# Kernel tuning notes

Measured on AMD Instinct MI355X. Metric: run time of the kernel, lower is better.

## Reference

```python
import jax, jax.numpy as jnp
import numpy as np

SEGMENT_LENGTHS = (768, 1536, 3072, 6144, 12288)
DILATED_RATIOS = (1, 2, 4, 8, 16)
NUM_HEADS = 12
NEG_INF = -1e9


def _layer_norm(x, g, b, eps=1e-5):
    mu = jnp.mean(x, axis=-1, keepdims=True)
    var = jnp.mean((x - mu) ** 2, axis=-1, keepdims=True)
    return (x - mu) * jax.lax.rsqrt(var + eps) * g + b


def _dilated_branch(q, k, v, w, r):
    # q,k,v: (B, L, H, Dh); segment length w, dilation ratio r (w % r == 0)
    B, L, H, Dh = q.shape
    Lp = -(-L // w) * w
    n, m = Lp // w, w // r
    gsz = -(-H // r)  # head-group size (heads padded up to a multiple of r in LongNet)
    offs = jnp.arange(H) // gsz  # per-head token offset within each r-block
    oh = jax.nn.one_hot(offs, r, dtype=q.dtype)  # (H, r)

    def gather(t):
        t = jnp.pad(t, ((0, 0), (0, Lp - L), (0, 0), (0, 0)))
        t = t.reshape(B, n, m, r, H, Dh)  # segments of w = m blocks of r
        return jnp.einsum('bnmrhd,hr->bnmhd', t, oh)  # each head picks its offset

    qi, ki, vi = gather(q), gather(k), gather(v)
    s = jnp.einsum('bnihd,bnjhd->bnhij', qi * (Dh ** -0.5), ki)  # (B,n,H,m,m)
    lse = jax.scipy.special.logsumexp(s, axis=-1)  # (B,n,H,m)
    o = jnp.einsum('bnhij,bnjhd->bnihd', jax.nn.softmax(s, axis=-1), vi)
    # scatter back to dense token positions; uncovered slots get 0 / -inf lse
    o_full = jnp.einsum('bnmhd,hr->bnmrhd', o, oh).reshape(B, Lp, H, Dh)
    lse = jnp.transpose(lse, (0, 1, 3, 2))  # (B,n,m,H)
    lse_full = jnp.where(oh.T[None, None, None] > 0, lse[:, :, :, None, :], NEG_INF)
    lse_full = lse_full.reshape(B, Lp, H)
    return o_full[:, :L], lse_full[:, :L]


def _dilated_attention(q, k, v):
    outs, lses = [], []
    for w, r in zip(SEGMENT_LENGTHS, DILATED_RATIOS):
        o, l = _dilated_branch(q, k, v, w, r)
        outs.append(o)
        lses.append(l)
    lse = jnp.stack(lses)  # (n_branch, B, L, H)
    wts = jnp.exp(lse - lse.max(0))
    wts = wts / wts.sum(0)  # softmax-combine branches by their lse (LongNet recombination)
    return (jnp.stack(outs) * wts[..., None]).sum(0)  # (B, L, H, Dh)


def _forward(x, patch_w, patch_b, cls_token, pos_embed,
             ln1_g, ln1_b, wq, bq, wk, bk, wv, bv, wo, bo,
             ln2_g, ln2_b, w1, b1, w2, b2, normf_g, normf_b, head_w, head_b):
    B, Cin, D, Hs, Ws = x.shape
    E = patch_w.shape[0]
    pd, ph, pw = patch_w.shape[2], patch_w.shape[3], patch_w.shape[4]
    # non-overlapping 3D patch embed (Conv3d with stride == kernel)
    xp = x.reshape(B, Cin, D // pd, pd, Hs // ph, ph, Ws // pw, pw)
    tok = jnp.einsum('bcxpyqzr,ecpqr->bxyze', xp, patch_w).reshape(B, -1, E) + patch_b
    tok = tok + pos_embed[:, 1:]
    cls = cls_token + pos_embed[:, :1]
    h = jnp.concatenate([jnp.broadcast_to(cls, (B, 1, E)), tok], axis=1)
    L = h.shape[1]
    Dh = E // NUM_HEADS
    depth = wq.shape[0]
    for i in range(depth):  # pre-LN transformer layers with LongNet dilated attention
        hn = _layer_norm(h, ln1_g[i], ln1_b[i])
        q = (hn @ wq[i] + bq[i]).reshape(B, L, NUM_HEADS, Dh)
        k = (hn @ wk[i] + bk[i]).reshape(B, L, NUM_HEADS, Dh)
        v = (hn @ wv[i] + bv[i]).reshape(B, L, NUM_HEADS, Dh)
        a = _dilated_attention(q, k, v).reshape(B, L, E)
        h = h + a @ wo[i] + bo[i]
        hn = _layer_norm(h, ln2_g[i], ln2_b[i])
        h = h + jax.nn.gelu(hn @ w1[i] + b1[i], approximate=False) @ w2[i] + b2[i]
    h = _layer_norm(h, normf_g, normf_b)
    return h[:, 0] @ head_w + head_b  # (B, num_classes)


def setup_inputs() -> dict:
    key = jax.random.key(0)
    ks = jax.random.split(key, 12)
    B, E, depth, ncls = 2, 768, 2, 1000
    D, Hs, Ws = 48, 256, 256
    N = (D // 4) * (Hs // 16) * (Ws // 16)  # 3072 patches
    f32 = jnp.float32
    s = 0.02
    return {
        'x': jax.random.normal(ks[0], (B, 1, D, Hs, Ws), f32),
        'patch_w': jax.random.normal(ks[1], (E, 1, 4, 16, 16), f32) * s,
        'patch_b': jnp.zeros((E,), f32),
        'cls_token': jax.random.normal(ks[2], (1, 1, E), f32) * s,
        'pos_embed': jax.random.normal(ks[3], (1, N + 1, E), f32) * s,
        'ln1_g': jnp.ones((depth, E), f32),
        'ln1_b': jnp.zeros((depth, E), f32),
        'wq': jax.random.normal(ks[4], (depth, E, E), f32) * s,
        'bq': jnp.zeros((depth, E), f32),
        'wk': jax.random.normal(ks[5], (depth, E, E), f32) * s,
        'bk': jnp.zeros((depth, E), f32),
        'wv': jax.random.normal(ks[6], (depth, E, E), f32) * s,
        'bv': jnp.zeros((depth, E), f32),
        'wo': jax.random.normal(ks[7], (depth, E, E), f32) * s,
        'bo': jnp.zeros((depth, E), f32),
        'ln2_g': jnp.ones((depth, E), f32),
        'ln2_b': jnp.zeros((depth, E), f32),
        'w1': jax.random.normal(ks[8], (depth, E, 4 * E), f32) * s,
        'b1': jnp.zeros((depth, 4 * E), f32),
        'w2': jax.random.normal(ks[9], (depth, 4 * E, E), f32) * s,
        'b2': jnp.zeros((depth, E), f32),
        'normf_g': jnp.ones((E,), f32),
        'normf_b': jnp.zeros((E,), f32),
        'head_w': jax.random.normal(ks[10], (E, ncls), f32) * s,
        'head_b': jnp.zeros((ncls,), f32),
    }


def reference(x, patch_w, patch_b, cls_token, pos_embed,
              ln1_g, ln1_b, wq, bq, wk, bk, wv, bv, wo, bo,
              ln2_g, ln2_b, w1, b1, w2, b2, normf_g, normf_b, head_w, head_b):
    return _forward(x, patch_w, patch_b, cls_token, pos_embed,
                    ln1_g, ln1_b, wq, bq, wk, bk, wv, bv, wo, bo,
                    ln2_g, ln2_b, w1, b1, w2, b2, normf_g, normf_b, head_w, head_b)
```

## Files before the change

### kernel.cpp

```cpp
#include <hip/hip_runtime.h>
#include <math.h>

#define TOK_L 3073
#define EMB 768
#define NH 12
#define DH 64
#define BATCH 2
#define QKVS 2304
#define HSZ ((size_t)BATCH * TOK_L * EMB)
#define MHC ((size_t)BATCH * TOK_L * NH)

typedef __bf16 bf16;
typedef __bf16 v8bf __attribute__((ext_vector_type(8)));
typedef __bf16 v4bf __attribute__((ext_vector_type(4)));
typedef float  v4f  __attribute__((ext_vector_type(4)));
typedef unsigned int v4u __attribute__((ext_vector_type(4)));

__device__ __forceinline__ v8bf zero8() {
    v8bf v;
    #pragma unroll
    for (int i = 0; i < 8; i++) v[i] = (bf16)0.f;
    return v;
}
__device__ __forceinline__ v4f zero4() {
    v4f v; v[0] = 0.f; v[1] = 0.f; v[2] = 0.f; v[3] = 0.f; return v;
}
__device__ __forceinline__ float gelu_f(float x) {
    return 0.5f * x * (1.0f + erff(x * 0.70710678118654752f));
}
__device__ __forceinline__ void gload16(const bf16* g, bf16* l) {
    __builtin_amdgcn_global_load_lds(
        (const __attribute__((address_space(1))) void*)g,
        (__attribute__((address_space(3))) void*)l, 16, 0, 0);
}

__device__ __forceinline__ void convT_tile(const float* __restrict__ src,
                                           bf16* __restrict__ dst,
                                           int K, int N, int tx, int ty)
{
    __shared__ float t[32][33];
    int n0 = tx * 32, k0 = ty * 32;
    int r = threadIdx.x >> 3, c4 = (threadIdx.x & 7) * 4;
    float4 v = *(const float4*)(src + (size_t)(k0 + r) * N + n0 + c4);
    t[r][c4 + 0] = v.x; t[r][c4 + 1] = v.y; t[r][c4 + 2] = v.z; t[r][c4 + 3] = v.w;
    __syncthreads();
    v4bf o;
    o[0] = (bf16)t[c4 + 0][r]; o[1] = (bf16)t[c4 + 1][r];
    o[2] = (bf16)t[c4 + 2][r]; o[3] = (bf16)t[c4 + 3][r];
    *(v4bf*)(dst + (size_t)(n0 + r) * K + k0 + c4) = o;
}

__global__ __launch_bounds__(256) void prep_weights(
    const float* __restrict__ wq, const float* __restrict__ wk,
    const float* __restrict__ wv, const float* __restrict__ wo,
    const float* __restrict__ w1, const float* __restrict__ w2,
    const float* __restrict__ patch_w,
    bf16* __restrict__ qkv_t0, bf16* __restrict__ wo_t0,
    bf16* __restrict__ w1_t, bf16* __restrict__ w2_t, bf16* __restrict__ pw_b)
{
    int bid = blockIdx.x;
    if (bid >= 13824) {
        int i = ((bid - 13824) * 256 + threadIdx.x) * 4;
        float4 v = *(const float4*)(patch_w + i);
        v4bf o; o[0] = (bf16)v.x; o[1] = (bf16)v.y; o[2] = (bf16)v.z; o[3] = (bf16)v.w;
        *(v4bf*)(pw_b + i) = o;
        return;
    }
    int layer = bid / 6912, t = bid % 6912;
    if (t < 1728) {
        int m = t / 576, tt = t % 576;
        const float* src = (m == 0 ? wq : m == 1 ? wk : wv) + (size_t)layer * 589824;
        bf16* dst = qkv_t0 + (size_t)layer * QKVS * 768 + (size_t)m * 589824;
        convT_tile(src, dst, 768, 768, tt % 24, tt / 24);
    } else if (t < 2304) {
        int tt = t - 1728;
        convT_tile(wo + (size_t)layer * 589824, wo_t0 + (size_t)layer * 589824,
                   768, 768, tt % 24, tt / 24);
    } else if (t < 4608) {
        int tt = t - 2304;
        convT_tile(w1 + (size_t)layer * 2359296, w1_t + (size_t)layer * 2359296,
                   768, 3072, tt % 96, tt / 96);
    } else {
        int tt = t - 4608;
        convT_tile(w2 + (size_t)layer * 2359296, w2_t + (size_t)layer * 2359296,
                   3072, 768, tt % 24, tt / 24);
    }
}

__global__ __launch_bounds__(256) void prep_small(const float* __restrict__ bq,
    const float* __restrict__ bk, const float* __restrict__ bv, float* __restrict__ d,
    const float* __restrict__ cls, const float* __restrict__ pos, float* __restrict__ h)
{
    int i = blockIdx.x * 256 + threadIdx.x;
    if (i < 2 * QKVS) {
        int layer = i / QKVS, j = i % QKVS;
        const float* s = (j < 768) ? bq : (j < 1536) ? bk : bv;
        d[i] = s[(size_t)layer * 768 + (j & 767)];
    }
    if (i < 2 * 768) {
        int b = i / 768, e = i % 768;
        h[(size_t)b * TOK_L * EMB + e] = cls[e] + pos[e];
    }
}

__global__ __launch_bounds__(256) void gather_patches(const float* __restrict__ x,
                                                      bf16* __restrict__ Xp) {
    int p = blockIdx.x;
    int b = p / 3072, pp = p % 3072;
    int px = pp >> 8, py = (pp >> 4) & 15, pz = pp & 15;
    for (int k = threadIdx.x; k < 1024; k += 256) {
        int pd = k >> 8, ph = (k >> 4) & 15, pw = k & 15;
        size_t src = ((size_t)(b * 48 + px * 4 + pd)) * 65536
                   + (size_t)(py * 16 + ph) * 256 + (size_t)(pz * 16 + pw);
        Xp[(size_t)p * 1024 + k] = (bf16)x[src];
    }
}

__device__ __forceinline__ void remap_tile(int NX, int MY, int G, int& xo, int& yo)
{
    int id = blockIdx.x + NX * blockIdx.y;
    int nwg = NX * MY;
    int xcd = id & 7, j = id >> 3;
    int q = nwg >> 3, r = nwg & 7;
    int n = xcd * q + (xcd < r ? xcd : r) + j;
    int full = MY / G;
    int bpg = NX * G;
    int nf = full * bpg;
    if (n < nf) {
        int gi = n / bpg, w = n - gi * bpg;
        int xi = w / G;
        xo = xi; yo = gi * G + (w - xi * G);
    } else {
        int t = MY - full * G;
        int w = n - nf;
        int xi = w / t;
        xo = xi; yo = full * G + (w - xi * t);
    }
}

template<int BN>
__global__ __launch_bounds__(256) void gemm_bf16(
    const bf16* __restrict__ A, const bf16* __restrict__ Bt,
    const float* __restrict__ bias, float* __restrict__ Cf,
    bf16* __restrict__ Cb, int M, int N, int K, int flags,
    const float* __restrict__ pos, int G)
{
    __shared__ bf16 As[2][128 * 32];
    __shared__ bf16 Bs[2][BN * 32];
    const int tid = threadIdx.x;
    const int lane = tid & 63, wid = tid >> 6;
    const int ln15 = lane & 15, q4 = lane >> 4;
    int xo, yo;
    remap_tile(gridDim.x, gridDim.y, G, xo, yo);
    const int m0 = yo * 128, n0 = xo * BN;
    const int wm = (wid & 1) * 64, wn = (wid >> 1) * (BN / 2);
    const int srow = lane >> 2;
    const int schunk = (lane & 3) * 8;
    const int NF = BN / 32;

    v4f acc[4][NF];
    #pragma unroll
    for (int i = 0; i < 4; i++)
        #pragma unroll
        for (int j = 0; j < NF; j++) acc[i][j] = zero4();

    const int NT = K >> 5;
    auto stage = [&](int kt, int bi) {
        const int k0 = kt << 5;
        #pragma unroll
        for (int i = 0; i < 2; i++) {
            int rg = wid * 32 + i * 16;
            int gm = m0 + rg + srow; if (gm >= M) gm = M - 1;
            gload16(A + (size_t)gm * K + k0 + schunk, &As[bi][rg * 32]);
        }
        if (BN == 128) {
            #pragma unroll
            for (int i = 0; i < 2; i++) {
                int rg = wid * 32 + i * 16;
                gload16(Bt + (size_t)(n0 + rg + srow) * K + k0 + schunk, &Bs[bi][rg * 32]);
            }
        } else {
            int rg = wid * 16;
            gload16(Bt + (size_t)(n0 + rg + srow) * K + k0 + schunk, &Bs[bi][rg * 32]);
        }
    };

    stage(0, 0);
    __syncthreads();

    for (int kt = 0; kt < NT; kt++) {
        const int cur = kt & 1;
        if (kt + 1 < NT) stage(kt + 1, cur ^ 1);
        v8bf af[4], bfr[NF];
        #pragma unroll
        for (int mt = 0; mt < 4; mt++)
            af[mt] = *(const v8bf*)(&As[cur][(wm + mt * 16 + ln15) * 32 + q4 * 8]);
        #pragma unroll
        for (int nt = 0; nt < NF; nt++)
            bfr[nt] = *(const v8bf*)(&Bs[cur][(wn + nt * 16 + ln15) * 32 + q4 * 8]);
        #pragma unroll
        for (int mt = 0; mt < 4; mt++)
            #pragma unroll
            for (int nt = 0; nt < NF; nt++)
                acc[mt][nt] = __builtin_amdgcn_mfma_f32_16x16x32_bf16(af[mt], bfr[nt], acc[mt][nt], 0, 0, 0);
        __syncthreads();
    }
    #pragma unroll
    for (int mt = 0; mt < 4; mt++) {
        #pragma unroll
        for (int nt = 0; nt < NF; nt++) {
            #pragma unroll
            for (int g = 0; g < 4; g++) {
                int row = m0 + wm + mt * 16 + q4 * 4 + g;
                if (row >= M) continue;
                int col = n0 + wn + nt * 16 + ln15;
                float v = acc[mt][nt][g] + bias[col];
                if (flags & 2) v = gelu_f(v);
                size_t crow;
                if (flags & 4) {
                    int rowp = row % 3072;
                    crow = (size_t)(row + row / 3072 + 1);
                    v += pos[(size_t)(rowp + 1) * EMB + col];
                } else crow = (size_t)row;
                size_t ci = crow * (size_t)N + col;
                if (flags & 8) Cb[ci] = (bf16)v;
                else { if (flags & 1) v += Cf[ci]; Cf[ci] = v; }
            }
        }
    }
}

__global__ __launch_bounds__(256) void layernorm_kernel(
    const float* __restrict__ x, const float* __restrict__ g,
    const float* __restrict__ bb, bf16* __restrict__ y, int nrows)
{
    int row = blockIdx.x;
    if (row >= nrows) return;
    int tid = threadIdx.x;
    const float* xr = x + (size_t)row * EMB;
    float v0 = xr[tid], v1 = xr[tid + 256], v2 = xr[tid + 512];
    __shared__ float red[256];
    red[tid] = v0 + v1 + v2;
    __syncthreads();
    for (int o = 128; o > 0; o >>= 1) { if (tid < o) red[tid] += red[tid + o]; __syncthreads(); }
    float mu = red[0] * (1.f / 768.f);
    __syncthreads();
    float d0 = v0 - mu, d1 = v1 - mu, d2 = v2 - mu;
    red[tid] = d0 * d0 + d1 * d1 + d2 * d2;
    __syncthreads();
    for (int o = 128; o > 0; o >>= 1) { if (tid < o) red[tid] += red[tid + o]; __syncthreads(); }
    float rs = rsqrtf(red[0] * (1.f / 768.f) + 1e-5f);
    bf16* yr = y + (size_t)row * EMB;
    yr[tid]       = (bf16)(d0 * rs * g[tid]       + bb[tid]);
    yr[tid + 256] = (bf16)(d1 * rs * g[tid + 256] + bb[tid + 256]);
    yr[tid + 512] = (bf16)(d2 * rs * g[tid + 512] + bb[tid + 512]);
}

__global__ __launch_bounds__(256) void pack_vt(const bf16* __restrict__ qkv,
                                               bf16* __restrict__ Vt)
{
    __shared__ bf16 t[64 * 65];
    int yy = blockIdx.y;
    int br, seg;
    if (yy < 5)       { br = 0; seg = yy; }
    else if (yy < 8)  { br = 1; seg = yy - 5; }
    else if (yy < 10) { br = 2; seg = yy - 8; }
    else if (yy == 10){ br = 3; seg = 0; }
    else              { br = 4; seg = 0; }
    const int r = 1 << br, w = 768 << br;
    const int gsz = (NH + r - 1) / r;
    const int bh = blockIdx.z;
    const int b = bh / NH, hd = bh % NH;
    const int off = hd / gsz;
    const int kbase = seg * w + off;
    const int kt = blockIdx.x;
    const int tid = threadIdx.x;
    const int dq = (tid & 7) * 8;
    #pragma unroll
    for (int p = 0; p < 2; p++) {
        int jl = (tid >> 3) + p * 32;
        int pk = kbase + (kt * 64 + jl) * r;
        v8bf val = (pk < TOK_L)
            ? *(const v8bf*)(qkv + (size_t)(b * TOK_L + pk) * QKVS + 1536 + hd * DH + dq)
            : zero8();
        #pragma unroll
        for (int i = 0; i < 8; i++) t[jl * 65 + dq + i] = val[i];
    }
    __syncthreads();
    #pragma unroll
    for (int p = 0; p < 2; p++) {
        int d = (tid >> 3) + p * 32;
        int kk = (tid & 7) * 8;
        v8bf o;
        #pragma unroll
        for (int i = 0; i < 8; i++) o[i] = t[(kk + i) * 65 + d];
        *(v8bf*)(Vt + ((size_t)(yy * 24 + bh) * 64 + d) * 768 + kt * 64 + kk) = o;
    }
}

__global__ __launch_bounds__(256) void attn_mfma(
    const bf16* __restrict__ qkv, const bf16* __restrict__ Vt,
    bf16* __restrict__ oac, bf16* __restrict__ obr, float* __restrict__ lse5)
{
    __shared__ bf16 kl[2 * 4096];
    const int tid = threadIdx.x;
    const int lane = tid & 63, wid = tid >> 6;
    const int ln15 = lane & 15, q4 = lane >> 4;
    const int bid = blockIdx.x;
    const int xcd = bid & 7, rest = bid >> 3;
    const int slot = rest / 6, t = rest - slot * 6;
    const int g = (slot << 3) | xcd;
    const int yy = g / 24, bh = g - yy * 24;
    int br, seg;
    if (yy < 5)       { br = 0; seg = yy; }
    else if (yy < 8)  { br = 1; seg = yy - 5; }
    else if (yy < 10) { br = 2; seg = yy - 8; }
    else if (yy == 10){ br = 3; seg = 0; }
    else              { br = 4; seg = 0; }
    const int r = 1 << br, w = 768 << br;
    const int gsz = (NH + r - 1) / r;
    const int b = bh / NH, hd = bh % NH;
    const int off = hd / gsz;
    const int sbase = seg * w + off;
    if (sbase + (t * 128) * r >= TOK_L) return;

    int n_valid = (TOK_L - sbase + r - 1) / r;
    if (n_valid > 768) n_valid = 768;
    const int kt_lim = (n_valid + 63) >> 6;
    const float pad_add = (float)(768 - n_valid);
    const int qoff = t * 128 + wid * 32;
    const bool wactive = (sbase + qoff * r) < TOK_L;

    const bf16* qb_ = qkv + hd * DH;
    const bf16* kb_ = qkv + 768 + hd * DH;

    const int swz = (ln15 & 7) * 8;

    auto stageK = [&](int ktv, int bufi) {
        #pragma unroll
        for (int p = 0; p < 2; p++) {
            int row = (tid >> 3) + p * 32;
            int pk = sbase + (ktv * 64 + row) * r;
            if (pk >= TOK_L) pk = 0;
            int colsw = ((tid & 7) ^ ((tid >> 3) & 7)) * 8;
            gload16(kb_ + (size_t)(b * TOK_L + pk) * QKVS + colsw,
                    kl + bufi * 4096 + wid * 512 + p * 2048);
        }
    };

    v8bf qf[2][2];
    #pragma unroll
    for (int mt = 0; mt < 2; mt++) {
        int pq = sbase + (qoff + mt * 16 + ln15) * r;
        #pragma unroll
        for (int ks = 0; ks < 2; ks++) {
            v8bf qv = (pq < TOK_L)
                ? *(const v8bf*)(qb_ + (size_t)(b * TOK_L + pq) * QKVS + ks * 32 + q4 * 8)
                : zero8();
            #pragma unroll
            for (int i = 0; i < 8; i++) qv[i] = (bf16)((float)qv[i] * 0.125f);
            qf[mt][ks] = qv;
        }
    }
    v4f o[2][4];
    float lsum[2];
    #pragma unroll
    for (int mt = 0; mt < 2; mt++) {
        lsum[mt] = 0.f;
        #pragma unroll
        for (int dt = 0; dt < 4; dt++) o[mt][dt] = zero4();
    }

    const bf16* vtb = Vt + (size_t)(yy * 24 + bh) * 64 * 768;

    stageK(0, 0);
    __syncthreads();

    for (int kt = 0; kt < kt_lim; kt++) {
        const int cur = kt & 1;
        if (kt + 1 < kt_lim) stageK(kt + 1, cur ^ 1);
        if (wactive) {
            const bf16* klc = kl + cur * 4096;
            v8bf kf[4][2];
            #pragma unroll
            for (int nt = 0; nt < 4; nt++)
                #pragma unroll
                for (int ks = 0; ks < 2; ks++)
                    kf[nt][ks] = *(const v8bf*)(klc + (nt * 16 + ln15) * 64
                                                + ((ks * 32 + q4 * 8) ^ swz));
            unsigned int paw[2][2][4];
            #pragma unroll
            for (int mt = 0; mt < 2; mt++) {
                v4f s[4];
                #pragma unroll
                for (int nt = 0; nt < 4; nt++) {
                    s[nt] = __builtin_amdgcn_mfma_f32_16x16x32_bf16(kf[nt][0], qf[mt][0], zero4(), 0, 0, 0);
                    s[nt] = __builtin_amdgcn_mfma_f32_16x16x32_bf16(kf[nt][1], qf[mt][1], s[nt], 0, 0, 0);
                }
                unsigned int W[4][2];
                float ls = 0.f;
                #pragma unroll
                for (int nt = 0; nt < 4; nt++) {
                    int kb = kt * 64 + nt * 16 + q4 * 4;
                    float p0 = (kb + 0 < n_valid) ? __expf(s[nt][0]) : 0.f;
                    float p1 = (kb + 1 < n_valid) ? __expf(s[nt][1]) : 0.f;
                    float p2 = (kb + 2 < n_valid) ? __expf(s[nt][2]) : 0.f;
                    float p3 = (kb + 3 < n_valid) ? __expf(s[nt][3]) : 0.f;
                    ls += (p0 + p1) + (p2 + p3);
                    asm("v_cvt_pk_bf16_f32 %0, %1, %2" : "=v"(W[nt][0]) : "v"(p0), "v"(p1));
                    asm("v_cvt_pk_bf16_f32 %0, %1, %2" : "=v"(W[nt][1]) : "v"(p2), "v"(p3));
                }
                lsum[mt] += ls;
                #pragma unroll
                for (int ks = 0; ks < 2; ks++) {
                    #pragma unroll
                    for (int h = 0; h < 2; h++) {
                        unsigned int a = W[2 * ks][h], c = W[2 * ks + 1][h];
                        asm("v_permlane32_swap_b32 %0, %1" : "+v"(a), "+v"(c));
                        asm("v_permlane16_swap_b32 %0, %1" : "+v"(a), "+v"(c));
                        paw[mt][ks][h]     = a;
                        paw[mt][ks][2 + h] = c;
                    }
                }
            }
            #pragma unroll
            for (int ks = 0; ks < 2; ks++) {
                v8bf vf[4];
                #pragma unroll
                for (int dt = 0; dt < 4; dt++)
                    vf[dt] = *(const v8bf*)(vtb + (size_t)(dt * 16 + ln15) * 768 + kt * 64 + ks * 32 + q4 * 8);
                #pragma unroll
                for (int mt = 0; mt < 2; mt++) {
                    v4u pw = { paw[mt][ks][0], paw[mt][ks][1], paw[mt][ks][2], paw[mt][ks][3] };
                    v8bf pa = __builtin_bit_cast(v8bf, pw);
                    #pragma unroll
                    for (int dt = 0; dt < 4; dt++)
                        o[mt][dt] = __builtin_amdgcn_mfma_f32_16x16x32_bf16(pa, vf[dt], o[mt][dt], 0, 0, 0);
                }
            }
        }
        __syncthreads();
    }
    if (!wactive) return;

    float lf[2];
    #pragma unroll
    for (int mt = 0; mt < 2; mt++) {
        float l = lsum[mt];
        l += __shfl_xor(l, 16, 64);
        l += __shfl_xor(l, 32, 64);
        l += pad_add;
        lf[mt] = l;
        if (q4 == 0) {
            int pq = sbase + (qoff + mt * 16 + ln15) * r;
            if (pq < TOK_L)
                lse5[(size_t)br * MHC + (size_t)(b * TOK_L + pq) * NH + hd] = __logf(l);
        }
    }

    bf16* od = (br == 0) ? oac : obr + (size_t)(br - 1) * HSZ;
    #pragma unroll
    for (int mt = 0; mt < 2; mt++) {
        #pragma unroll
        for (int g2 = 0; g2 < 4; g2++) {
            float l = __shfl(lf[mt], q4 * 4 + g2, 64);
            int row = mt * 16 + q4 * 4 + g2;
            int pq = sbase + (qoff + row) * r;
            if (pq >= TOK_L) continue;
            float linv = 1.f / l;
            #pragma unroll
            for (int dt = 0; dt < 4; dt++)
                od[(size_t)(b * TOK_L + pq) * EMB + hd * DH + dt * 16 + ln15] =
                    (bf16)(o[mt][dt][g2] * linv);
        }
    }
}

__global__ __launch_bounds__(256) void attn_combine(
    const bf16* __restrict__ oac, const bf16* __restrict__ obr,
    const float* __restrict__ lse5, bf16* __restrict__ outb)
{
    size_t e = (size_t)blockIdx.x * 256 + threadIdx.x;
    if (e >= HSZ) return;
    size_t g = e >> 6;
    int h = (int)(g % NH);
    int p = (int)((g / NH) % TOK_L);
    float l0 = lse5[g];
    float m = l0;
    float lv[4];
    bool cov[4];
    #pragma unroll
    for (int j = 0; j < 4; j++) {
        int r = 2 << j;
        int gsz = (NH + r - 1) / r;
        cov[j] = ((p & (r - 1)) == (h / gsz));
        if (cov[j]) {
            lv[j] = lse5[(size_t)(j + 1) * MHC + g];
            m = fmaxf(m, lv[j]);
        }
    }
    float w0 = __expf(l0 - m);
    float wsum = w0;
    float acc = w0 * (float)oac[e];
    #pragma unroll
    for (int j = 0; j < 4; j++) {
        if (cov[j]) {
            float wj = __expf(lv[j] - m);
            wsum += wj;
            acc = fmaf(wj, (float)obr[(size_t)j * HSZ + e], acc);
        }
    }
    outb[e] = (bf16)(acc / wsum);
}

__global__ __launch_bounds__(256) void head_kernel(
    const bf16* __restrict__ hn, const float* __restrict__ hw,
    const float* __restrict__ hb, float* __restrict__ out)
{
    int b = blockIdx.y;
    int c = blockIdx.x * 256 + threadIdx.x;
    __shared__ float srow[EMB];
    for (int e = threadIdx.x; e < EMB; e += 256)
        srow[e] = (float)hn[(size_t)b * TOK_L * EMB + e];
    __syncthreads();
    if (c < 1000) {
        float acc = hb[c];
        for (int e = 0; e < EMB; e++)
            acc = fmaf(srow[e], hw[(size_t)e * 1000 + c], acc);
        out[b * 1000 + c] = acc;
    }
}

extern "C" void kernel_launch(void* const* d_in, const int* in_sizes, int n_in,
                              void* d_out, int out_size, void* d_ws, size_t ws_size,
                              hipStream_t stream)
{
    const float* x       = (const float*)d_in[0];
    const float* patch_w = (const float*)d_in[1];
    const float* patch_b = (const float*)d_in[2];
    const float* cls_tok = (const float*)d_in[3];
    const float* pos_emb = (const float*)d_in[4];
    const float* ln1_g   = (const float*)d_in[5];
    const float* ln1_b   = (const float*)d_in[6];
    const float* wq      = (const float*)d_in[7];
    const float* bq      = (const float*)d_in[8];
    const float* wk      = (const float*)d_in[9];
    const float* bk      = (const float*)d_in[10];
    const float* wv      = (const float*)d_in[11];
    const float* bv      = (const float*)d_in[12];
    const float* wo      = (const float*)d_in[13];
    const float* bo      = (const float*)d_in[14];
    const float* ln2_g   = (const float*)d_in[15];
    const float* ln2_b   = (const float*)d_in[16];
    const float* w1      = (const float*)d_in[17];
    const float* b1      = (const float*)d_in[18];
    const float* w2      = (const float*)d_in[19];
    const float* b2      = (const float*)d_in[20];
    const float* normf_g = (const float*)d_in[21];
    const float* normf_b = (const float*)d_in[22];
    const float* head_w  = (const float*)d_in[23];
    const float* head_b  = (const float*)d_in[24];
    float* out = (float*)d_out;

    char* wp = (char*)d_ws;
    auto alloc = [&](size_t bytes) { char* r = wp; wp += (bytes + 255) & ~(size_t)255; return r; };
    float* h    = (float*)alloc(HSZ * 4);
    bf16*  hn   = (bf16*)alloc(HSZ * 2);
    bf16*  QKV  = (bf16*)alloc((size_t)BATCH * TOK_L * QKVS * 2);
    bf16*  oac  = (bf16*)alloc(HSZ * 2);
    float* lse5 = (float*)alloc(5 * MHC * 4);
    bf16*  Vt   = (bf16*)alloc((size_t)12 * 24 * 64 * 768 * 2);
    bf16*  mid  = (bf16*)alloc(4 * HSZ * 2);
    bf16*  obr  = mid;
    bf16*  Xp   = mid;

    bf16*  qkv_t0 = (bf16*)alloc((size_t)2 * QKVS * 768 * 2);
    bf16*  wo_t0  = (bf16*)alloc((size_t)2 * 768 * 768 * 2);
    bf16*  w1_t   = (bf16*)alloc((size_t)2 * 3072 * 768 * 2);
    bf16*  w2_t   = (bf16*)alloc((size_t)2 * 768 * 3072 * 2);
    bf16*  pw_b   = (bf16*)alloc((size_t)768 * 1024 * 2);
    float* bqkv   = (float*)alloc((size_t)2 * QKVS * 4);

    const int M = BATCH * TOK_L;
    const int MT = (M + 127) / 128;

    prep_weights<<<dim3(14592), 256, 0, stream>>>(wq, wk, wv, wo, w1, w2, patch_w,
                                                  qkv_t0, wo_t0, w1_t, w2_t, pw_b);
    prep_small<<<dim3(18), 256, 0, stream>>>(bq, bk, bv, bqkv, cls_tok, pos_emb, h);

    gather_patches<<<dim3(BATCH * 3072), 256, 0, stream>>>(x, Xp);
    gemm_bf16<64><<<dim3(12, 48), 256, 0, stream>>>(Xp, pw_b, patch_b, h, nullptr,
                                                    BATCH * 3072, 768, 1024, 4, pos_emb, 8);

    for (int layer = 0; layer < 2; layer++) {
        size_t bOff  = (size_t)layer * 768;
        size_t b1Off = (size_t)layer * 3072;
        bf16* qt   = qkv_t0 + (size_t)layer * QKVS * 768;
        bf16* wo_t = wo_t0 + (size_t)layer * 589824;

        layernorm_kernel<<<dim3(M), 256, 0, stream>>>(h, ln1_g + bOff, ln1_b + bOff, hn, M);
        gemm_bf16<128><<<dim3(18, MT), 256, 0, stream>>>(hn, qt, bqkv + (size_t)layer * QKVS,
                                                         nullptr, QKV, M, QKVS, 768, 8, nullptr, 8);

        pack_vt<<<dim3(12, 12, 24), 256, 0, stream>>>(QKV, Vt);
        attn_mfma<<<dim3(1728), 256, 0, stream>>>(QKV, Vt, oac, obr, lse5);
        attn_combine<<<dim3((unsigned)((HSZ + 255) / 256)), 256, 0, stream>>>(oac, obr, lse5, hn);

        gemm_bf16<64><<<dim3(12, MT), 256, 0, stream>>>(hn, wo_t, bo + bOff, h, nullptr,
                                                        M, 768, 768, 1, nullptr, 8);

        layernorm_kernel<<<dim3(M), 256, 0, stream>>>(h, ln2_g + bOff, ln2_b + bOff, hn, M);
        gemm_bf16<128><<<dim3(24, MT), 256, 0, stream>>>(hn, w1_t + (size_t)layer * 2359296, b1 + b1Off,
                                                         nullptr, mid, M, 3072, 768, 8 | 2, nullptr, 8);
        gemm_bf16<64><<<dim3(12, MT), 256, 0, stream>>>(mid, w2_t + (size_t)layer * 2359296, b2 + bOff,
                                                        h, nullptr, M, 768, 3072, 1, nullptr, 4);
    }

    layernorm_kernel<<<dim3(M), 256, 0, stream>>>(h, normf_g, normf_b, hn, M);
    head_kernel<<<dim3(4, BATCH), 256, 0, stream>>>(hn, head_w, head_b, out);
}
```

Before: 972.6 us.

## Double GEMM M-tile to 256 rows and replace syncthreads with explicit vmcnt waits

The bf16 GEMM tile grows from 128 to 256 rows. Each wave now owns 128x64 (BN=128) or 64x64 (BN=64) of the output, which raises MFMA work per shared-memory fragment load and halves grid rows. The loop drops __syncthreads and instead waits on outstanding global loads with s_waitcnt vmcnt counts, then issues raw s_barrier with sched barriers, so the next tile's prefetch overlaps the current compute. The larger tile doubles LDS use and raises accumulator register pressure, and halving the number of blocks may underfill the GPU's CUs. The hand-counted vmcnt values must match the number of loads each stage issues.

```diff
diff --git a/kernel.cpp b/kernel.cpp
--- a/kernel.cpp
+++ b/kernel.cpp
@@ -145,31 +145,32 @@
     bf16* __restrict__ Cb, int M, int N, int K, int flags,
     const float* __restrict__ pos, int G)
 {
-    __shared__ bf16 As[2][128 * 32];
+    __shared__ bf16 As[2][256 * 32];
     __shared__ bf16 Bs[2][BN * 32];
     const int tid = threadIdx.x;
     const int lane = tid & 63, wid = tid >> 6;
     const int ln15 = lane & 15, q4 = lane >> 4;
     int xo, yo;
     remap_tile(gridDim.x, gridDim.y, G, xo, yo);
-    const int m0 = yo * 128, n0 = xo * BN;
-    const int wm = (wid & 1) * 64, wn = (wid >> 1) * (BN / 2);
+    const int m0 = yo * 256, n0 = xo * BN;
+    constexpr int MTW = (BN == 128) ? 8 : 4;
+    const int wm = (BN == 128) ? (wid & 1) * 128 : wid * 64;
+    const int wn = (BN == 128) ? (wid >> 1) * 64 : 0;
     const int srow = lane >> 2;
     const int schunk = (lane & 3) * 8;
-    const int NF = BN / 32;
-
-    v4f acc[4][NF];
-    #pragma unroll
-    for (int i = 0; i < 4; i++)
-        #pragma unroll
-        for (int j = 0; j < NF; j++) acc[i][j] = zero4();
+
+    v4f acc[MTW][4];
+    #pragma unroll
+    for (int i = 0; i < MTW; i++)
+        #pragma unroll
+        for (int j = 0; j < 4; j++) acc[i][j] = zero4();
 
     const int NT = K >> 5;
     auto stage = [&](int kt, int bi) {
         const int k0 = kt << 5;
         #pragma unroll
-        for (int i = 0; i < 2; i++) {
-            int rg = wid * 32 + i * 16;
+        for (int i = 0; i < 4; i++) {
+            int rg = wid * 64 + i * 16;
             int gm = m0 + rg + srow; if (gm >= M) gm = M - 1;
             gload16(A + (size_t)gm * K + k0 + schunk, &As[bi][rg * 32]);
         }
@@ -186,29 +187,38 @@
     };
 
     stage(0, 0);
-    __syncthreads();
 
     for (int kt = 0; kt < NT; kt++) {
         const int cur = kt & 1;
-        if (kt + 1 < NT) stage(kt + 1, cur ^ 1);
-        v8bf af[4], bfr[NF];
-        #pragma unroll
-        for (int mt = 0; mt < 4; mt++)
+        if (kt + 1 < NT) {
+            stage(kt + 1, cur ^ 1);
+            if (BN == 128) asm volatile("s_waitcnt vmcnt(6)" ::: "memory");
+            else           asm volatile("s_waitcnt vmcnt(5)" ::: "memory");
+        } else {
+            asm volatile("s_waitcnt vmcnt(0)" ::: "memory");
+        }
+        __builtin_amdgcn_sched_barrier(0);
+        __builtin_amdgcn_s_barrier();
+        __builtin_amdgcn_sched_barrier(0);
+
+        v8bf af[MTW], bfr[4];
+        #pragma unroll
+        for (int mt = 0; mt < MTW; mt++)
             af[mt] = *(const v8bf*)(&As[cur][(wm + mt * 16 + ln15) * 32 + q4 * 8]);
         #pragma unroll
-        for (int nt = 0; nt < NF; nt++)
+        for (int nt = 0; nt < 4; nt++)
             bfr[nt] = *(const v8bf*)(&Bs[cur][(wn + nt * 16 + ln15) * 32 + q4 * 8]);
         #pragma unroll
-        for (int mt = 0; mt < 4; mt++)
-            #pragma unroll
-            for (int nt = 0; nt < NF; nt++)
+        for (int mt = 0; mt < MTW; mt++)
+            #pragma unroll
+            for (int nt = 0; nt < 4; nt++)
                 acc[mt][nt] = __builtin_amdgcn_mfma_f32_16x16x32_bf16(af[mt], bfr[nt], acc[mt][nt], 0, 0, 0);
-        __syncthreads();
-    }
-    #pragma unroll
-    for (int mt = 0; mt < 4; mt++) {
-        #pragma unroll
-        for (int nt = 0; nt < NF; nt++) {
+        __builtin_amdgcn_s_barrier();
+    }
+    #pragma unroll
+    for (int mt = 0; mt < MTW; mt++) {
+        #pragma unroll
+        for (int nt = 0; nt < 4; nt++) {
             #pragma unroll
             for (int g = 0; g < 4; g++) {
                 int row = m0 + wm + mt * 16 + q4 * 4 + g;
@@ -582,15 +592,15 @@
     float* bqkv   = (float*)alloc((size_t)2 * QKVS * 4);
 
     const int M = BATCH * TOK_L;
-    const int MT = (M + 127) / 128;
+    const int MT2 = (M + 255) / 256;
 
     prep_weights<<<dim3(14592), 256, 0, stream>>>(wq, wk, wv, wo, w1, w2, patch_w,
                                                   qkv_t0, wo_t0, w1_t, w2_t, pw_b);
     prep_small<<<dim3(18), 256, 0, stream>>>(bq, bk, bv, bqkv, cls_tok, pos_emb, h);
 
     gather_patches<<<dim3(BATCH * 3072), 256, 0, stream>>>(x, Xp);
-    gemm_bf16<64><<<dim3(12, 48), 256, 0, stream>>>(Xp, pw_b, patch_b, h, nullptr,
-                                                    BATCH * 3072, 768, 1024, 4, pos_emb, 8);
+    gemm_bf16<64><<<dim3(12, 24), 256, 0, stream>>>(Xp, pw_b, patch_b, h, nullptr,
+                                                    BATCH * 3072, 768, 1024, 4, pos_emb, 4);
 
     for (int layer = 0; layer < 2; layer++) {
         size_t bOff  = (size_t)layer * 768;
@@ -599,21 +609,21 @@
         bf16* wo_t = wo_t0 + (size_t)layer * 589824;
 
         layernorm_kernel<<<dim3(M), 256, 0, stream>>>(h, ln1_g + bOff, ln1_b + bOff, hn, M);
-        gemm_bf16<128><<<dim3(18, MT), 256, 0, stream>>>(hn, qt, bqkv + (size_t)layer * QKVS,
-                                                         nullptr, QKV, M, QKVS, 768, 8, nullptr, 8);
+        gemm_bf16<128><<<dim3(18, MT2), 256, 0, stream>>>(hn, qt, bqkv + (size_t)layer * QKVS,
+                                                          nullptr, QKV, M, QKVS, 768, 8, nullptr, 4);
 
         pack_vt<<<dim3(12, 12, 24), 256, 0, stream>>>(QKV, Vt);
         attn_mfma<<<dim3(1728), 256, 0, stream>>>(QKV, Vt, oac, obr, lse5);
         attn_combine<<<dim3((unsigned)((HSZ + 255) / 256)), 256, 0, stream>>>(oac, obr, lse5, hn);
 
-        gemm_bf16<64><<<dim3(12, MT), 256, 0, stream>>>(hn, wo_t, bo + bOff, h, nullptr,
-                                                        M, 768, 768, 1, nullptr, 8);
+        gemm_bf16<64><<<dim3(12, MT2), 256, 0, stream>>>(hn, wo_t, bo + bOff, h, nullptr,
+                                                         M, 768, 768, 1, nullptr, 4);
 
         layernorm_kernel<<<dim3(M), 256, 0, stream>>>(h, ln2_g + bOff, ln2_b + bOff, hn, M);
-        gemm_bf16<128><<<dim3(24, MT), 256, 0, stream>>>(hn, w1_t + (size_t)layer * 2359296, b1 + b1Off,
-                                                         nullptr, mid, M, 3072, 768, 8 | 2, nullptr, 8);
-        gemm_bf16<64><<<dim3(12, MT), 256, 0, stream>>>(mid, w2_t + (size_t)layer * 2359296, b2 + bOff,
-                                                        h, nullptr, M, 768, 3072, 1, nullptr, 4);
+        gemm_bf16<128><<<dim3(24, MT2), 256, 0, stream>>>(hn, w1_t + (size_t)layer * 2359296, b1 + b1Off,
+                                                          nullptr, mid, M, 3072, 768, 8 | 2, nullptr, 4);
+        gemm_bf16<64><<<dim3(12, MT2), 256, 0, stream>>>(mid, w2_t + (size_t)layer * 2359296, b2 + bOff,
+                                                         h, nullptr, M, 768, 3072, 1, nullptr, 2);
     }
 
     layernorm_kernel<<<dim3(M), 256, 0, stream>>>(h, normf_g, normf_b, hn, M);
```

Measured after the change: 1.389 ms. 42.8% more time.
